# Kernel tuning notes

Hardware: AMD Instinct MI355X
Metric: run time of the kernel (lower is better)

Reference implementation:

```python
import jax, jax.numpy as jnp
import numpy as np

# Static trigram-LM trie configuration (uniform branching K per node).
V_ = 32000; N_ = 3; K_ = 32; S_ = 32; SOS_ = 0; B_ = 32; L_ = 8
U_ = V_ + 1
N_BI = V_ * K_                    # number of bigram nodes
O_ = U_ + N_BI + 1                # offsets/logbs length (bigram block + sentinel)
N_TRI = N_BI * K_                 # number of trigram leaves
G_ = N_TRI
P_ = O_ + G_                      # logps length


def _build_trie():
    """Valid CSR-style flattened trie: children of node at position q live at
    [offsets[q]+q, offsets[q+1]+q+1); every node has exactly K children with
    sorted token ids 0..K-1. ids[p-U_] is the token id of node at position p."""
    rng = np.random.default_rng(0)
    offsets = np.empty(O_, np.int64)
    # unigram v's children occupy positions [U_+v*K_, U_+(v+1)*K_)
    offsets[:U_] = U_ + np.arange(U_) * (K_ - 1)
    # bigram j (position U_+j) children occupy [O_+j*K_, O_+(j+1)*K_)
    offsets[U_:] = (O_ - U_) + np.arange(N_BI + 1) * (K_ - 1)
    ids = np.empty(P_ - U_, np.int32)
    ids[:N_BI] = np.arange(N_BI) % K_       # bigram node token ids
    ids[N_BI] = 0                           # sentinel slot at position O_-1
    ids[N_BI + 1:] = np.arange(N_TRI) % K_  # trigram leaf token ids
    logps = (-rng.uniform(0.1, 10.0, P_)).astype(np.float32)
    logbs = (-rng.uniform(0.01, 2.0, O_)).astype(np.float32)
    return offsets.astype(np.int32), ids, logps, logbs


def setup_inputs() -> dict:
    key = jax.random.key(0)
    k1, k2 = jax.random.split(key)
    offsets, ids, logps, logbs = _build_trie()
    # tokens in [0, 2K): half of them miss in the trie -> exercises backoff path
    hist = jax.random.randint(k1, (L_, B_), 0, 2 * K_, dtype=jnp.int32)
    hidx = jax.random.randint(k2, (B_,), 0, L_, dtype=jnp.int32)
    return {"hist": hist, "hidx": hidx, "offsets": jnp.asarray(offsets),
            "ids": jnp.asarray(ids), "logps": jnp.asarray(logps),
            "logbs": jnp.asarray(logbs), "sos": SOS_, "V": V_, "N": N_,
            "G": G_, "S": S_}


def reference(hist, hidx, offsets, ids, logps, logbs, sos, V, N, G, S):
    B = hist.shape[1]
    M = B * V
    O = offsets.shape[0]
    P = logps.shape[0]
    shift = 0 if 0 <= sos < V else 1
    U = V + shift + 1 % N
    if N == 1:
        return jnp.broadcast_to(logps[:V], (B, V))
    # Always left-pad N-1 sos tokens (equivalent to torch's rem padding; the
    # subsequent window gather makes extra padding harmless).
    pad = N - 1
    hist = jnp.concatenate([jnp.full((pad, B), sos, hist.dtype), hist])
    hidx = hidx + pad
    # context = the N-1 tokens at positions hidx-(N-1) .. hidx-1, per batch
    pos = hidx[None, :] - (N - 1) + jnp.arange(N - 1)[:, None]   # (N-1, B)
    ctx = jnp.take_along_axis(hist, pos, axis=0)                  # (N-1, B)
    if shift:
        ctx = jnp.where(ctx == sos, V, ctx)
    ctx = ctx.astype(ids.dtype)
    srange = jnp.arange(S)
    # first M entries: candidate words v per batch; last B: context pointer
    desc = jnp.concatenate([jnp.tile(jnp.arange(V, dtype=jnp.int32), B),
                            ctx[-1].astype(jnp.int32)])
    last_logps = jnp.tile(logps[:V], B)                           # (M,)
    last_backoffs = jnp.repeat(logbs[desc[M:]], V)                # (M,)
    found = jnp.ones(M + B, bool)
    for n in range(1, N):
        hist_n = jnp.concatenate([jnp.repeat(ctx[-n], V), ctx[-min(n + 1, N - 1)]])
        desc_starts = offsets[desc] + desc
        desc_ends = offsets[desc + 1] + desc + 1
        pos_desc = desc_starts[:, None] + srange[None, :]         # (M+B, S)
        ext = desc_ends[:, None] > pos_desc
        ids_ = ids[jnp.minimum(pos_desc, P - 1) - U]
        ext = ext & (hist_n[:, None] == ids_)
        found = ext.any(1) & found
        desc = jnp.where(found, jnp.where(ext, pos_desc, 0).sum(1), desc)
        logps_desc = logps[desc[:M]]
        if n == N - 1:
            cur_backoffs = jnp.zeros_like(last_backoffs)
        else:
            cur_backoffs = jnp.repeat(
                jnp.where(found[M:], logbs[jnp.minimum(desc[M:], O - 1)], 0.0), V)
        clobber = jnp.isfinite(logps_desc) & found[:M]
        cur_logps = jnp.where(clobber, logps_desc,
                              last_logps + cur_backoffs + last_backoffs)
        last_backoffs = jnp.where(clobber, cur_backoffs, 0.0)
        last_logps = jnp.where(jnp.repeat(hidx >= n, V), cur_logps, last_logps)
    return last_logps.reshape(B, V)
```

## Files before the change

### kernel.cpp

```cpp
#include <hip/hip_runtime.h>


#define MAXN 8

struct PerB {
  int   ctx[MAXN];
  float bo[MAXN];
  float b1;
  int   hp;
};

__device__ __forceinline__ bool find_child(const int* __restrict__ offsets,
                                           const int* __restrict__ ids,
                                           int q, int t, int U, int P, int S,
                                           int* pos_out) {
  int start = offsets[q] + q;
  int end   = offsets[q + 1] + q + 1;
  int n = end - start;
  if (n > S) n = S;
  if (n <= 0) return false;
  int j = (t < n - 1) ? t : (n - 1);
  if (j < 0) j = 0;
  int x = ids[min(start + j, P - 1) - U];
  if (x == t) { *pos_out = start + j; return true; }
  if (x < t) return false;
  int lo = 0, hi = j - 1;
  while (lo < hi) {
    int mid = (lo + hi) >> 1;
    int xm = ids[min(start + mid, P - 1) - U];
    if (xm < t) lo = mid + 1; else hi = mid;
  }
  if (lo < j) {
    int xm = ids[min(start + lo, P - 1) - U];
    if (xm == t) { *pos_out = start + lo; return true; }
  }
  return false;
}

__global__ void lm_prep(const int* __restrict__ hist, const int* __restrict__ hidx,
                        const int* __restrict__ offsets, const int* __restrict__ ids,
                        const float* __restrict__ logbs,
                        const int* __restrict__ sos_p, const int* __restrict__ N_p,
                        const int* __restrict__ S_p,
                        PerB* __restrict__ pb, int V, int B, int L, int O, int P) {
  int b = blockIdx.x * blockDim.x + threadIdx.x;
  if (b >= B) return;
  int sos = *sos_p, N = *N_p, S = *S_p;
  if (N <= 1) return;
  int shift = (0 <= sos && sos < V) ? 0 : 1;
  int U = V + shift + 1 % N;
  int pad = N - 1;
  int hp = hidx[b] + pad;
  PerB o;
  o.hp = hp;
  for (int k = 0; k < N - 1; ++k) {
    int r = hp - (N - 1) + k;
    int tok = (r < pad) ? sos : hist[(r - pad) * B + b];
    if (shift && tok == sos) tok = V;
    o.ctx[k] = tok;
  }
  o.b1 = logbs[o.ctx[N - 2]];
  int desc = o.ctx[N - 2];
  bool found = true;
  for (int n = 1; n <= N - 2; ++n) {
    int t = o.ctx[(N - 1) - min(n + 1, N - 1)];
    if (found) {
      int pos;
      found = find_child(offsets, ids, desc, t, U, P, S, &pos);
      if (found) desc = pos;
    }
    o.bo[n] = found ? logbs[min(desc, O - 1)] : 0.0f;
  }
  pb[b] = o;
}

__device__ __forceinline__ float score_v(const int* __restrict__ offsets,
                                         const int* __restrict__ ids,
                                         const float* __restrict__ logps,
                                         const PerB* __restrict__ pbb,
                                         int v, float lp0,
                                         int N, int U, int O, int P, int S) {
  float last_lp = lp0;
  float last_bo = pbb->b1;
  int hp = pbb->hp;
  int desc = v;
  bool found = true;
  float cur_lp = lp0;
#pragma unroll
  for (int n = 1; n <= N - 1; ++n) {
    int t = pbb->ctx[(N - 1) - n];
    if (found) {
      int pos;
      found = find_child(offsets, ids, desc, t, U, P, S, &pos);
      if (found) { desc = pos; cur_lp = logps[desc]; }
    }
    float cur_bo = (n == N - 1) ? 0.0f : pbb->bo[n];
    bool clobber = isfinite(cur_lp) && found;
    float newlp = clobber ? cur_lp : (last_lp + cur_bo + last_bo);
    last_bo = clobber ? cur_bo : 0.0f;
    if (hp >= n) last_lp = newlp;
  }
  return last_lp;
}

__global__ void __launch_bounds__(256)
lm_main(const int* __restrict__ offsets, const int* __restrict__ ids,
        const float* __restrict__ logps, const float* __restrict__ logbs,
        const int* __restrict__ sos_p, const int* __restrict__ N_p,
        const int* __restrict__ S_p,
        const PerB* __restrict__ pb, float* __restrict__ out,
        int V, int B, int O, int P) {
  int v = blockIdx.x * blockDim.x + threadIdx.x;
  int b = blockIdx.y;
  if (v >= V) return;
  int N = *N_p;
  float lp0 = logps[v];
  size_t oi = (size_t)b * (size_t)V + (size_t)v;
  if (N <= 1) { out[oi] = lp0; return; }
  int S = *S_p;
  int sos = *sos_p;
  int shift = (0 <= sos && sos < V) ? 0 : 1;
  int U = V + shift + 1 % N;
  const PerB* pbb = pb + b;
  float r;
  if (N == 3) {
    r = score_v(offsets, ids, logps, pbb, v, lp0, 3, U, O, P, S);
  } else {
    r = score_v(offsets, ids, logps, pbb, v, lp0, N, U, O, P, S);
  }
  out[oi] = r;
}

extern "C" void kernel_launch(void* const* d_in, const int* in_sizes, int n_in,
                              void* d_out, int out_size, void* d_ws, size_t ws_size,
                              hipStream_t stream) {
  const int*   hist    = (const int*)d_in[0];
  const int*   hidx    = (const int*)d_in[1];
  const int*   offsets = (const int*)d_in[2];
  const int*   ids     = (const int*)d_in[3];
  const float* logps   = (const float*)d_in[4];
  const float* logbs   = (const float*)d_in[5];
  const int*   sos_p   = (const int*)d_in[6];
  const int*   N_p     = (const int*)d_in[8];
  const int*   S_p     = (const int*)d_in[10];

  int B = in_sizes[1];
  int L = in_sizes[0] / B;
  int O = in_sizes[2];
  int P = in_sizes[4];
  int V = out_size / B;
  float* out = (float*)d_out;
  PerB* pb = (PerB*)d_ws;

  lm_prep<<<dim3((B + 63) / 64), dim3(64), 0, stream>>>(
      hist, hidx, offsets, ids, logbs, sos_p, N_p, S_p, pb, V, B, L, O, P);

  dim3 grid((V + 255) / 256, B);
  lm_main<<<grid, dim3(256), 0, stream>>>(
      offsets, ids, logps, logbs, sos_p, N_p, S_p, pb, out, V, B, O, P);
}
```

Baseline: 295.6 us.

## Batch 16 histories per thread and cache per-unigram children in LDS

```diff
diff --git a/kernel.cpp b/kernel.cpp
--- a/kernel.cpp
+++ b/kernel.cpp
@@ -1,7 +1,11 @@
 #include <hip/hip_runtime.h>
+#include <math.h>
 
 
 #define MAXN 8
+#define BG   16
+#define WI   37
+#define WO   41
 
 struct PerB {
   int   ctx[MAXN];
@@ -86,7 +90,6 @@
   int desc = v;
   bool found = true;
   float cur_lp = lp0;
-#pragma unroll
   for (int n = 1; n <= N - 1; ++n) {
     int t = pbb->ctx[(N - 1) - n];
     if (found) {
@@ -103,32 +106,180 @@
   return last_lp;
 }
 
-__global__ void __launch_bounds__(256)
-lm_main(const int* __restrict__ offsets, const int* __restrict__ ids,
-        const float* __restrict__ logps, const float* __restrict__ logbs,
-        const int* __restrict__ sos_p, const int* __restrict__ N_p,
-        const int* __restrict__ S_p,
-        const PerB* __restrict__ pb, float* __restrict__ out,
-        int V, int B, int O, int P) {
-  int v = blockIdx.x * blockDim.x + threadIdx.x;
-  int b = blockIdx.y;
+__global__ void __launch_bounds__(64)
+lm_main2(const int* __restrict__ offsets, const int* __restrict__ ids,
+         const float* __restrict__ logps,
+         const int* __restrict__ sos_p, const int* __restrict__ N_p,
+         const int* __restrict__ S_p,
+         const PerB* __restrict__ pb, float* __restrict__ out,
+         int V, int B, int O, int P) {
+  __shared__ int   s_t1[BG], s_t0[BG], s_hp[BG];
+  __shared__ float s_bo1[BG], s_b1[BG];
+  __shared__ int   ids_w[64 * WI];
+  __shared__ int   off_w[64 * WO];
+
+  const int tid = threadIdx.x;
+  const int v   = blockIdx.x * 64 + tid;
+  const int b0  = blockIdx.y * BG;
+  const int N = *N_p, S = *S_p, sos = *sos_p;
+  const int Nc = (N > 0) ? N : 1;
+  const int shift = (0 <= sos && sos < V) ? 0 : 1;
+  const int U = V + shift + 1 % Nc;
+
+  const bool fast = (N == 3) && (S == 32);
+
+  if (!fast) {
+    if (v < V) {
+      float lp0 = logps[v];
+      if (N <= 1) {
+        for (int i = 0; i < BG; ++i) {
+          int b = b0 + i;
+          if (b < B) out[(size_t)b * V + v] = lp0;
+        }
+      } else {
+        for (int i = 0; i < BG; ++i) {
+          int b = b0 + i;
+          if (b < B)
+            out[(size_t)b * V + v] = score_v(offsets, ids, logps, pb + b, v,
+                                             lp0, N, U, O, P, S);
+        }
+      }
+    }
+    return;
+  }
+
+  if (tid < BG) {
+    int b = b0 + tid;
+    if (b < B) {
+      const PerB* q = pb + b;
+      s_t1[tid]  = q->ctx[1];
+      s_t0[tid]  = q->ctx[0];
+      s_bo1[tid] = q->bo[1];
+      s_b1[tid]  = q->b1;
+      s_hp[tid]  = q->hp;
+    }
+  }
+  __syncthreads();
   if (v >= V) return;
-  int N = *N_p;
+
+  const int idsN = P - U;
   float lp0 = logps[v];
-  size_t oi = (size_t)b * (size_t)V + (size_t)v;
-  if (N <= 1) { out[oi] = lp0; return; }
-  int S = *S_p;
-  int sos = *sos_p;
-  int shift = (0 <= sos && sos < V) ? 0 : 1;
-  int U = V + shift + 1 % N;
-  const PerB* pbb = pb + b;
-  float r;
-  if (N == 3) {
-    r = score_v(offsets, ids, logps, pbb, v, lp0, 3, U, O, P, S);
+  int ov  = offsets[v];
+  int ov1 = offsets[v + 1];
+  int start1 = ov + v;
+  int n1 = ov1 + 1 - ov;
+  if (n1 > 32) n1 = 32;
+
+  int* myids = ids_w + tid * WI;
+  int* myoff = off_w + tid * WO;
+  int aidx0 = start1 - U;
+  int sh_i = 0, sh_o = 0;
+  bool vec_ok = (start1 >= 0) && (aidx0 >= 0) &&
+                (((aidx0 & ~3) + 36) <= idsN) &&
+                (((start1 & ~3) + 40) <= O);
+  if (vec_ok) {
+    int ab = aidx0 & ~3;
+    sh_i = aidx0 - ab;
+    const int4* ip = (const int4*)(ids + ab);
+#pragma unroll
+    for (int k = 0; k < 9; ++k) {
+      int4 t = ip[k];
+      myids[4 * k + 0] = t.x; myids[4 * k + 1] = t.y;
+      myids[4 * k + 2] = t.z; myids[4 * k + 3] = t.w;
+    }
+    int ob = start1 & ~3;
+    sh_o = start1 - ob;
+    const int4* op = (const int4*)(offsets + ob);
+#pragma unroll
+    for (int k = 0; k < 10; ++k) {
+      int4 t = op[k];
+      myoff[4 * k + 0] = t.x; myoff[4 * k + 1] = t.y;
+      myoff[4 * k + 2] = t.z; myoff[4 * k + 3] = t.w;
+    }
   } else {
-    r = score_v(offsets, ids, logps, pbb, v, lp0, N, U, O, P, S);
-  }
-  out[oi] = r;
+    for (int j = 0; j < 34; ++j) {
+      int ii = min(start1 + j, P - 1) - U;
+      ii = max(0, min(ii, idsN - 1));
+      myids[j] = ids[ii];
+      int oo = max(0, min(start1 + j, O - 1));
+      myoff[j] = offsets[oo];
+    }
+  }
+
+#pragma unroll
+  for (int i = 0; i < BG; ++i) {
+    int b = b0 + i;
+    if (b >= B) continue;
+    int   t1 = s_t1[i], t0 = s_t0[i], hp = s_hp[i];
+    float bo1 = s_bo1[i], last_bo = s_b1[i];
+    float last_lp = lp0;
+
+    bool found = false;
+    int j1 = 0;
+    if (n1 > 0) {
+      int jj = (t1 < n1 - 1) ? t1 : (n1 - 1);
+      if (jj < 0) jj = 0;
+      int x = myids[sh_i + jj];
+      if (x == t1) { found = true; j1 = jj; }
+      else if (x > t1) {
+        int lo = 0, hi = jj - 1;
+        while (lo < hi) {
+          int mid = (lo + hi) >> 1;
+          if (myids[sh_i + mid] < t1) lo = mid + 1; else hi = mid;
+        }
+        if (lo < jj && myids[sh_i + lo] == t1) { found = true; j1 = lo; }
+      }
+    }
+    int c1 = start1 + j1;
+    float lp1 = found ? logps[min(c1, P - 1)] : lp0;
+
+    {
+      bool clob = found && isfinite(lp1);
+      float nl = clob ? lp1 : (last_lp + bo1 + last_bo);
+      last_bo = clob ? bo1 : 0.0f;
+      if (hp >= 1) last_lp = nl;
+    }
+
+    if (found) {
+      int o1 = myoff[sh_o + j1];
+      int o2 = myoff[sh_o + j1 + 1];
+      int start2 = o1 + c1;
+      int n2 = o2 + 1 - o1;
+      if (n2 > 32) n2 = 32;
+      bool f2 = false;
+      float lp2 = 0.0f;
+      if (n2 > 0) {
+        int jj = (t0 < n2 - 1) ? t0 : (n2 - 1);
+        if (jj < 0) jj = 0;
+        int c2 = start2 + jj;
+        int cc = min(c2, P - 1);
+        int ii = max(0, min(cc - U, idsN - 1));
+        int   x2  = ids[ii];
+        float sp2 = logps[cc];
+        if (x2 == t0) { f2 = true; lp2 = sp2; }
+        else if (x2 > t0) {
+          int lo = 0, hi = jj - 1;
+          while (lo < hi) {
+            int mid = (lo + hi) >> 1;
+            int im = max(0, min(min(start2 + mid, P - 1) - U, idsN - 1));
+            if (ids[im] < t0) lo = mid + 1; else hi = mid;
+          }
+          if (lo < jj) {
+            int il = max(0, min(min(start2 + lo, P - 1) - U, idsN - 1));
+            if (ids[il] == t0) { f2 = true; lp2 = logps[min(start2 + lo, P - 1)]; }
+          }
+        }
+      }
+      bool clob2 = f2 && isfinite(lp2);
+      float nl2 = clob2 ? lp2 : (last_lp + last_bo);
+      if (hp >= 2) last_lp = nl2;
+    } else {
+      float nl2 = last_lp + last_bo;
+      if (hp >= 2) last_lp = nl2;
+    }
+
+    out[(size_t)b * V + v] = last_lp;
+  }
 }
 
 extern "C" void kernel_launch(void* const* d_in, const int* in_sizes, int n_in,
@@ -155,7 +306,7 @@
   lm_prep<<<dim3((B + 63) / 64), dim3(64), 0, stream>>>(
       hist, hidx, offsets, ids, logbs, sos_p, N_p, S_p, pb, V, B, L, O, P);
 
-  dim3 grid((V + 255) / 256, B);
-  lm_main<<<grid, dim3(256), 0, stream>>>(
-      offsets, ids, logps, logbs, sos_p, N_p, S_p, pb, out, V, B, O, P);
-}
+  dim3 grid((V + 63) / 64, (B + BG - 1) / BG);
+  lm_main2<<<grid, dim3(64), 0, stream>>>(
+      offsets, ids, logps, sos_p, N_p, S_p, pb, out, V, B, O, P);
+}
```

Measured after the change: 278.9 us. 1.06x faster.
